# Performance work log

Hardware: AMD Instinct MI355X
Metric: run time of the kernel (lower is better)

The kernel has to match this reference:

```python
import jax, jax.numpy as jnp
import numpy as np
from jax import lax

BN_EPS = 1e-5

def _tern(w):
    # TWN-style ternarization with straight-through estimator
    d = 0.7 * jnp.mean(jnp.abs(w))
    q = jnp.where(jnp.abs(w) > d, jnp.sign(w), jnp.zeros_like(w))
    return w + lax.stop_gradient(q - w)

def _conv(x, w, b):
    y = lax.conv_general_dilated(x, _tern(w), (1, 1), 'SAME',
                                 dimension_numbers=('NCHW', 'OIHW', 'NCHW'))
    return y + b[None, :, None, None]

def _bn4(x, g, b, m, v):
    inv = g * lax.rsqrt(v + BN_EPS)
    return (x - m[None, :, None, None]) * inv[None, :, None, None] + b[None, :, None, None]

def _bn2(x, g, b, m, v):
    return (x - m) * (g * lax.rsqrt(v + BN_EPS)) + b

def _pool(x):
    return lax.reduce_window(x, -jnp.inf, lax.max, (1, 1, 2, 2), (1, 1, 2, 2), 'VALID')


def setup_inputs() -> dict:
    key = jax.random.key(0)
    ks = jax.random.split(key, 8)
    f = jnp.float32
    d = {}
    d['x'] = jax.random.normal(ks[0], (1024, 1, 28, 28), f)
    wshapes = {'w1': (32, 1, 3, 3), 'w2': (64, 32, 3, 3), 'w3': (128, 64, 3, 3),
               'w4': (128, 128, 3, 3), 'wf1': (256, 6272), 'wf2': (128, 256), 'wf3': (10, 128)}
    for i, (n, s) in enumerate(wshapes.items()):
        d[n] = jax.random.normal(ks[i + 1], s, f) * 0.1
    for n, c in [('1', 32), ('2', 64), ('3', 128), ('4', 128)]:
        d['b' + n] = jnp.zeros((c,), f)
        d['g' + n] = jnp.ones((c,), f)
        d['be' + n] = jnp.zeros((c,), f)
        d['m' + n] = jnp.zeros((c,), f)
        d['v' + n] = jnp.ones((c,), f)
    for n, c in [('f1', 256), ('f2', 128)]:
        d['b' + n] = jnp.zeros((c,), f)
        d['g' + n] = jnp.ones((c,), f)
        d['be' + n] = jnp.zeros((c,), f)
        d['m' + n] = jnp.zeros((c,), f)
        d['v' + n] = jnp.ones((c,), f)
    d['bf3'] = jnp.zeros((10,), f)
    return d


def reference(x, w1, b1, g1, be1, m1, v1, w2, b2, g2, be2, m2, v2,
              w3, b3, g3, be3, m3, v3, w4, b4, g4, be4, m4, v4,
              wf1, bf1, gf1, bef1, mf1, vf1, wf2, bf2, gf2, bef2, mf2, vf2,
              wf3, bf3):
    h = jax.nn.relu(_bn4(_conv(x, w1, b1), g1, be1, m1, v1))
    h = jax.nn.relu(_bn4(_conv(h, w2, b2), g2, be2, m2, v2))
    h = _pool(h)                                  # [B,64,14,14]
    h = jax.nn.relu(_bn4(_conv(h, w3, b3), g3, be3, m3, v3))
    h = jax.nn.relu(_bn4(_conv(h, w4, b4), g4, be4, m4, v4))
    h = _pool(h)                                  # [B,128,7,7]
    h = h.reshape(h.shape[0], -1)                 # [B,6272]
    h = jax.nn.relu(_bn2(h @ _tern(wf1).T + bf1, gf1, bef1, mf1, vf1))
    h = jax.nn.relu(_bn2(h @ _tern(wf2).T + bf2, gf2, bef2, mf2, vf2))
    return h @ _tern(wf3).T + bf3                 # [B,10] logits
```

## Files before the change

### kernel.cpp

```cpp
#include <hip/hip_runtime.h>
#include <hip/hip_bf16.h>

#define BN_EPS 1e-5f

typedef __attribute__((ext_vector_type(8))) short bf16x8;
typedef __attribute__((ext_vector_type(4))) float f32x4;
typedef unsigned short u16;
typedef unsigned int u32;

__device__ __forceinline__ void load16(const void* g, void* l) {
    __builtin_amdgcn_global_load_lds((const __attribute__((address_space(1))) void*)g,
                                     (__attribute__((address_space(3))) void*)l, 16, 0, 0);
}
__device__ __forceinline__ u16 f2b(float v) {
    __hip_bfloat16 h = __float2bfloat16(v);
    return *reinterpret_cast<u16*>(&h);
}
__device__ __forceinline__ float ternq(float x, float d) {
    return (fabsf(x) > d) ? (x > 0.f ? 1.f : -1.f) : 0.f;
}

constexpr size_t ALGN(size_t x) { return (x + 255) & ~(size_t)255; }
constexpr size_t O_SUMS = 0;
constexpr size_t O_W1R  = 256;
constexpr size_t O_WF2Q = ALGN(O_W1R + 288 * 4);
constexpr size_t O_WF3Q = ALGN(O_WF2Q + 32768 * 4);
constexpr size_t O_BQ2  = ALGN(O_WF3Q + 1280 * 4);
constexpr size_t O_BQ3  = ALGN(O_BQ2 + 64 * 288 * 2);
constexpr size_t O_BQ4  = ALGN(O_BQ3 + 128 * 576 * 2);
constexpr size_t O_BQF1 = ALGN(O_BQ4 + 128 * 1152 * 2);
constexpr size_t O_F1   = ALGN(O_BQF1 + (size_t)256 * 6272 * 2);
constexpr size_t O_F2   = ALGN(O_F1 + 1024 * 256 * 4);
constexpr size_t O_ACT1 = ALGN(O_F2 + 1024 * 128 * 4);
constexpr size_t O_ACT2 = ALGN(O_ACT1 + (size_t)1024 * 900 * 32 * 2);
constexpr size_t O_ACT3 = ALGN(O_ACT2 + (size_t)1024 * 256 * 64 * 2);
constexpr size_t O_ACT4 = ALGN(O_ACT3 + (size_t)1024 * 256 * 128 * 2);

__global__ void zero_sums(float* s) { if (threadIdx.x < 8) s[threadIdx.x] = 0.f; }

__device__ void absmean_seg(const float* __restrict__ w, int n4, float* __restrict__ sum,
                            int b0, int nb) {
    __shared__ float sm[256];
    float s = 0.f;
    for (int i = b0 * 256 + threadIdx.x; i < n4; i += nb * 256) {
        float4 v = ((const float4*)w)[i];
        s += fabsf(v.x) + fabsf(v.y) + fabsf(v.z) + fabsf(v.w);
    }
    sm[threadIdx.x] = s;
    __syncthreads();
    for (int o = 128; o > 0; o >>= 1) {
        if (threadIdx.x < o) sm[threadIdx.x] += sm[threadIdx.x + o];
        __syncthreads();
    }
    if (threadIdx.x == 0) atomicAdd(sum, sm[0]);
}

__global__ void absmean_all(const float* w1, const float* w2, const float* w3, const float* w4,
                            const float* wf1, const float* wf2, const float* wf3, float* sums) {
    int b = blockIdx.x;
    if (b < 160)      absmean_seg(wf1, 401408, sums + 4, b, 160);
    else if (b < 192) absmean_seg(w4, 36864, sums + 3, b - 160, 32);
    else if (b < 208) absmean_seg(w3, 18432, sums + 2, b - 192, 16);
    else if (b < 216) absmean_seg(w2, 4608, sums + 1, b - 208, 8);
    else if (b < 224) absmean_seg(wf2, 8192, sums + 5, b - 216, 8);
    else if (b < 225) absmean_seg(w1, 72, sums + 0, 0, 1);
    else              absmean_seg(wf3, 320, sums + 6, 0, 1);
}

__device__ void tern_conv_seg(const float* __restrict__ w, float d, u16* __restrict__ bq,
                              int COUT, int CIN, int b0, int nb) {
    int N = COUT * CIN * 9;
    for (int i = b0 * 256 + threadIdx.x; i < N; i += nb * 256) {
        float q = ternq(w[i], d);
        int co = i / (CIN * 9), r = i % (CIN * 9);
        int ci = r / 9, tap = r % 9;
        bq[(size_t)co * CIN * 9 + tap * CIN + ci] = f2b(q);
    }
}
__device__ void tern_conv_prime_seg(const float* __restrict__ w, float d, u16* __restrict__ bqp,
                                    int CIN, int b0, int nb) {
    int N = 128 * CIN * 9;
    for (int i = b0 * 256 + threadIdx.x; i < N; i += nb * 256) {
        float q = ternq(w[i], d);
        int co = i / (CIN * 9), r = i % (CIN * 9);
        int ci = r / 9, tap = r % 9;
        int k = tap * CIN + ci;
        int s = k >> 5, qd = (k & 31) >> 3, e = k & 7;
        int lane = qd * 16 + (co & 15), nt = co >> 4;
        bqp[((size_t)(s * 8 + nt) * 64 + lane) * 8 + e] = f2b(q);
    }
}
__device__ void tern_f32_seg(const float* __restrict__ w, float d, float* __restrict__ wq,
                             int N, int b0, int nb) {
    for (int i = b0 * 256 + threadIdx.x; i < N; i += nb * 256) wq[i] = ternq(w[i], d);
}

__global__ void tern_all(const float* w1, const float* w2, const float* w3, const float* w4,
                         const float* wf1, const float* wf2, const float* wf3,
                         const float* __restrict__ sums,
                         float* w1r, u16* bq2, u16* bq3p, u16* bq4p, u16* bqf1,
                         float* wf2q, float* wf3q) {
    int b = blockIdx.x;
    if (b < 1) {
        tern_f32_seg(w1, 0.7f * sums[0] / 288.f, w1r, 288, 0, 1);
    } else if (b < 9) {
        tern_conv_seg(w2, 0.7f * sums[1] / 18432.f, bq2, 64, 32, b - 1, 8);
    } else if (b < 41) {
        tern_conv_prime_seg(w3, 0.7f * sums[2] / 73728.f, bq3p, 64, b - 9, 32);
    } else if (b < 105) {
        tern_conv_prime_seg(w4, 0.7f * sums[3] / 147456.f, bq4p, 128, b - 41, 64);
    } else if (b < 617) {
        float d = 0.7f * sums[4] / 1605632.f;
        for (int i = (b - 105) * 256 + threadIdx.x; i < 1605632; i += 512 * 256) {
            float q = ternq(wf1[i], d);
            int j = i / 6272, k = i % 6272;
            int c = k / 49, s = k % 49;
            bqf1[(size_t)j * 6272 + s * 128 + c] = f2b(q);
        }
    } else if (b < 633) {
        tern_f32_seg(wf2, 0.7f * sums[5] / 32768.f, wf2q, 32768, b - 617, 16);
    } else {
        tern_f32_seg(wf3, 0.7f * sums[6] / 1280.f, wf3q, 1280, 0, 1);
    }
}

__global__ void zero_f1(float* f1) {
    ((float4*)f1)[blockIdx.x * 256 + threadIdx.x] = make_float4(0.f, 0.f, 0.f, 0.f);
}

__global__ __launch_bounds__(256)
void conv1_direct(const float* __restrict__ x, const float* __restrict__ w1r,
                  const float* __restrict__ bias, const float* __restrict__ gam,
                  const float* __restrict__ bet, const float* __restrict__ mu,
                  const float* __restrict__ var, u16* __restrict__ out) {
    __shared__ float xs[784];
    __shared__ float wsh[288];
    __shared__ float scl[32], sft[32];
    const int n = blockIdx.x, tid = threadIdx.x;
    for (int i = tid; i < 784; i += 256) xs[i] = x[(size_t)n * 784 + i];
    for (int i = tid; i < 288; i += 256) wsh[i] = w1r[i];
    if (tid < 32) {
        float s = gam[tid] * rsqrtf(var[tid] + BN_EPS);
        scl[tid] = s;
        sft[tid] = (bias[tid] - mu[tid]) * s + bet[tid];
    }
    __syncthreads();
    for (int p = tid; p < 784; p += 256) {
        int y = p / 28, xx = p % 28;
        float patch[9];
#pragma unroll
        for (int dy = 0; dy < 3; ++dy)
#pragma unroll
            for (int dx = 0; dx < 3; ++dx) {
                int gy = y + dy - 1, gx = xx + dx - 1;
                patch[dy * 3 + dx] = (gy >= 0 && gy < 28 && gx >= 0 && gx < 28) ? xs[gy * 28 + gx] : 0.f;
            }
        u32 pk[16];
#pragma unroll
        for (int co = 0; co < 32; co += 2) {
            float s0 = 0.f, s1 = 0.f;
#pragma unroll
            for (int t = 0; t < 9; ++t) {
                s0 += wsh[co * 9 + t] * patch[t];
                s1 += wsh[(co + 1) * 9 + t] * patch[t];
            }
            float v0 = fmaxf(s0 * scl[co] + sft[co], 0.f);
            float v1 = fmaxf(s1 * scl[co + 1] + sft[co + 1], 0.f);
            pk[co >> 1] = ((u32)f2b(v1) << 16) | (u32)f2b(v0);
        }
        size_t base = ((size_t)(n * 30 + y + 1) * 30 + (xx + 1)) * 32;
#pragma unroll
        for (int q = 0; q < 4; ++q) ((uint4*)(out + base))[q] = ((uint4*)pk)[q];
    }
}

template<int C, int HP, int HV>
__global__ void border_zero(u16* __restrict__ buf) {
    constexpr int NB = 2 * HP + 2 * HV;
    constexpr int CG = C / 8;
    int i = blockIdx.x * blockDim.x + threadIdx.x;
    if (i >= 1024 * NB * CG) return;
    int cg = i % CG, r = i / CG;
    int b = r % NB, n = r / NB;
    int py, px;
    if (b < HP)               { py = 0;                  px = b; }
    else if (b < 2 * HP)      { py = HP - 1;             px = b - HP; }
    else if (b < 2 * HP + HV) { py = b - 2 * HP + 1;     px = 0; }
    else                      { py = b - 2 * HP - HV + 1; px = HP - 1; }
    size_t off = ((size_t)(n * HP + py) * HP + px) * C + cg * 8;
    *(uint4*)(buf + off) = make_uint4(0, 0, 0, 0);
}

template<int CIN, int BN, int HV, int HP, int G, bool POOL, bool PADOUT>
__global__ __launch_bounds__(256)
void convgemm(const u16* __restrict__ act, const u16* __restrict__ bq,
              const float* __restrict__ bias, const float* __restrict__ gam,
              const float* __restrict__ bet, const float* __restrict__ mu,
              const float* __restrict__ var, u16* __restrict__ out) {
    constexpr int BM = 128;
    constexpr int K = 9 * CIN;
    constexpr int S = K / (32 * G);
    constexpr int TPC = CIN / 32;
    constexpr int NT = BN / 32;
    constexpr int RB = BN / 64;
    constexpr int HO = HV / 2;
    constexpr int PP = POOL ? HO * HO : HV * HV;

    __shared__ __align__(16) u16 Alds[G][BM * 32];
    __shared__ __align__(16) u16 Blds[G][BN * 32];
    __shared__ int rowA[BM];
    __shared__ int rowO[BM];
    __shared__ float scl[BN], sft[BN];

    const int tid = threadIdx.x;
    const int m0 = blockIdx.x * BM;

    for (int t = tid; t < BM; t += 256) {
        int base;
        if (POOL) {
            int p = (m0 >> 2) + (t >> 2), q = t & 3;
            int n = p / PP, rr = p % PP;
            int oy = rr / HO, ox = rr % HO;
            int y = oy * 2 + (q >> 1), x = ox * 2 + (q & 1);
            base = ((n * HP + y) * HP + x) * CIN;
        } else {
            int m = m0 + t;
            int n = m / PP, rr = m % PP;
            int y = rr / HV, x = rr % HV;
            base = ((n * HP + y) * HP + x) * CIN;
        }
        rowA[t] = base;
    }
    if (POOL) {
        if (tid < 32) {
            int p = (m0 >> 2) + tid;
            int n = p / PP, rr = p % PP;
            int oy = rr / HO, ox = rr % HO;
            rowO[tid] = PADOUT ? ((n * 16 + oy + 1) * 16 + ox + 1) * BN : p * BN;
        }
    } else {
        for (int t = tid; t < BM; t += 256) {
            int m = m0 + t;
            int n = m / PP, rr = m % PP;
            int y = rr / HV, x = rr % HV;
            rowO[t] = PADOUT ? ((n * 16 + y + 1) * 16 + x + 1) * BN : m * BN;
        }
    }
    if (tid < BN) {
        float s = gam[tid] * rsqrtf(var[tid] + BN_EPS);
        scl[tid] = s;
        sft[tid] = (bias[tid] - mu[tid]) * s + bet[tid];
    }
    __syncthreads();

    int arow[2];
    arow[0] = rowA[(tid >> 6) * 16 + (tid & 15)];
    arow[1] = rowA[64 + (tid >> 6) * 16 + (tid & 15)];
    const int chunkb = ((tid >> 4) & 3) * 16;
    const int bco = (tid >> 6) * 16 + (tid & 15);
    const char* actb = (const char*)act;
    const char* bqb  = (const char*)bq;

    const int wave = tid >> 6, lane = tid & 63;
    const int wm = wave & 1, wn = wave >> 1;
    const int fr16 = lane * 16;

    f32x4 acc[4][NT] = {};

    for (int s = 0; s < S; ++s) {
#pragma unroll
        for (int j = 0; j < G; ++j) {
            int g = s * G + j;
            int tap = g / TPC, cio = (g % TPC) * 32;
            int dy = tap / 3, dx = tap % 3;
            int toffb = ((dy * HP + dx) * CIN + cio) * 2;
            char* Al = (char*)Alds[j];
#pragma unroll
            for (int r = 0; r < 2; ++r)
                load16(actb + (size_t)arow[r] * 2 + toffb + chunkb, Al + r * 4096 + tid * 16);
            char* Bl = (char*)Blds[j];
            int bkob = g * 64 + chunkb;
#pragma unroll
            for (int r = 0; r < RB; ++r)
                load16(bqb + (size_t)(r * 64 + bco) * K * 2 + bkob, Bl + r * 4096 + tid * 16);
        }
        __syncthreads();
#pragma unroll
        for (int j = 0; j < G; ++j) {
            const char* Al = (const char*)Alds[j];
            const char* Bl = (const char*)Blds[j];
            bf16x8 af[4], bf[NT];
#pragma unroll
            for (int mt = 0; mt < 4; ++mt)
                af[mt] = *(const bf16x8*)(Al + (wm * 4 + mt) * 1024 + fr16);
#pragma unroll
            for (int nt = 0; nt < NT; ++nt)
                bf[nt] = *(const bf16x8*)(Bl + (wn * NT + nt) * 1024 + fr16);
#pragma unroll
            for (int mt = 0; mt < 4; ++mt)
#pragma unroll
                for (int nt = 0; nt < NT; ++nt)
                    acc[mt][nt] = __builtin_amdgcn_mfma_f32_16x16x32_bf16(af[mt], bf[nt], acc[mt][nt], 0, 0, 0);
        }
        __syncthreads();
    }

    const int fr = lane & 15, quad = lane >> 4;
    if (POOL) {
#pragma unroll
        for (int mt = 0; mt < 4; ++mt) {
            int pl = wm * 16 + mt * 4 + quad;
            int ob = rowO[pl];
#pragma unroll
            for (int nt = 0; nt < NT; ++nt) {
                int col = wn * (NT * 16) + nt * 16 + fr;
                float sc = scl[col], sh = sft[col];
                f32x4 a = acc[mt][nt];
                float v0 = a[0] * sc + sh, v1 = a[1] * sc + sh;
                float v2 = a[2] * sc + sh, v3 = a[3] * sc + sh;
                float mx = fmaxf(fmaxf(v0, v1), fmaxf(v2, v3));
                out[(size_t)ob + col] = f2b(fmaxf(mx, 0.f));
            }
        }
    } else {
#pragma unroll
        for (int mt = 0; mt < 4; ++mt) {
            int rb = wm * 64 + mt * 16 + quad * 4;
            int o0 = rowO[rb], o1 = rowO[rb + 1], o2 = rowO[rb + 2], o3 = rowO[rb + 3];
#pragma unroll
            for (int nt = 0; nt < NT; ++nt) {
                int col = wn * (NT * 16) + nt * 16 + fr;
                float sc = scl[col], sh = sft[col];
                f32x4 a = acc[mt][nt];
                out[(size_t)o0 + col] = f2b(fmaxf(a[0] * sc + sh, 0.f));
                out[(size_t)o1 + col] = f2b(fmaxf(a[1] * sc + sh, 0.f));
                out[(size_t)o2 + col] = f2b(fmaxf(a[2] * sc + sh, 0.f));
                out[(size_t)o3 + col] = f2b(fmaxf(a[3] * sc + sh, 0.f));
            }
        }
    }
}

__global__ __launch_bounds__(256)
void conv34(const u16* __restrict__ act2p, const u16* __restrict__ b3p, const u16* __restrict__ b4p,
            const float* __restrict__ b3, const float* __restrict__ g3, const float* __restrict__ be3,
            const float* __restrict__ m3, const float* __restrict__ v3,
            const float* __restrict__ b4, const float* __restrict__ g4, const float* __restrict__ be4,
            const float* __restrict__ m4, const float* __restrict__ v4,
            u16* __restrict__ out) {
    __shared__ __align__(16) u16 Xs[32768];

    const int tid = threadIdx.x;
    const int n = blockIdx.x;
    const int wave = tid >> 6, lane = tid & 63;
    const int wm = wave & 1, wn = wave >> 1;
    const int fr = lane & 15, quad = lane >> 4;
    char* X = (char*)Xs;

    float scl3[4], sft3[4], scl4[4], sft4[4];
#pragma unroll
    for (int nt = 0; nt < 4; ++nt) {
        int c = wn * 64 + nt * 16 + fr;
        float s = g3[c] * rsqrtf(v3[c] + BN_EPS);
        scl3[nt] = s; sft3[nt] = (b3[c] - m3[c]) * s + be3[c];
        s = g4[c] * rsqrtf(v4[c] + BN_EPS);
        scl4[nt] = s; sft4[nt] = (b4[c] - m4[c]) * s + be4[c];
    }

    {
        const uint4* src = (const uint4*)(act2p + (size_t)n * 16384);
#pragma unroll
        for (int it = 0; it < 8; ++it) {
            int i = it * 256 + tid;
            int r = i >> 3, c = i & 7;
            uint4 v = src[i];
            *(uint4*)(X + r * 128 + ((c ^ (r & 7)) * 16)) = v;
        }
    }
    __syncthreads();

    int r0a[7];
#pragma unroll
    for (int mtl = 0; mtl < 7; ++mtl) {
        int g = wm * 7 + mtl + 1;
        int pxc = min(max(fr, 1), 14);
        r0a[mtl] = (g - 1) * 16 + (pxc - 1);
    }
    f32x4 acc[7][4] = {};
    const char* B3 = (const char*)b3p;
#pragma unroll 3
    for (int s = 0; s < 18; ++s) {
        int tap = s >> 1;
        int rdel = (tap / 3) * 16 + tap % 3;
        int cs = (s & 1) * 4;
        bf16x8 af[7], bf[4];
#pragma unroll
        for (int mtl = 0; mtl < 7; ++mtl) {
            int r = r0a[mtl] + rdel;
            int pos = (cs + quad) ^ (r & 7);
            af[mtl] = *(const bf16x8*)(X + r * 128 + pos * 16);
        }
#pragma unroll
        for (int nt = 0; nt < 4; ++nt)
            bf[nt] = *(const bf16x8*)(B3 + ((size_t)((s * 8 + wn * 4 + nt) * 64 + lane)) * 16);
#pragma unroll
        for (int mtl = 0; mtl < 7; ++mtl)
#pragma unroll
            for (int nt = 0; nt < 4; ++nt)
                acc[mtl][nt] = __builtin_amdgcn_mfma_f32_16x16x32_bf16(af[mtl], bf[nt], acc[mtl][nt], 0, 0, 0);
    }
    __syncthreads();

    for (int t = tid; t < 60 * 16; t += 256) {
        int j = t & 15, b = t >> 4;
        int m = (b < 16) ? b : (b < 32) ? 240 + (b - 16) : (b < 46) ? (b - 31) * 16 : (b - 45) * 16 + 15;
        *(uint4*)(X + m * 256 + j * 16) = make_uint4(0, 0, 0, 0);
    }
#pragma unroll
    for (int mtl = 0; mtl < 7; ++mtl) {
        int g = wm * 7 + mtl + 1;
#pragma unroll
        for (int nt = 0; nt < 4; ++nt) {
            int col = wn * 64 + nt * 16 + fr;
            int c = col >> 3;
            f32x4 a = acc[mtl][nt];
#pragma unroll
            for (int j = 0; j < 4; ++j) {
                int px = quad * 4 + j;
                if (px >= 1 && px <= 14) {
                    int m = g * 16 + px;
                    float v = fmaxf(a[j] * scl3[nt] + sft3[nt], 0.f);
                    *(u16*)(X + m * 256 + ((c ^ (m & 15)) * 16) + (col & 7) * 2) = f2b(v);
                }
            }
        }
    }
    __syncthreads();

    int r0b[7];
#pragma unroll
    for (int mtl = 0; mtl < 7; ++mtl) {
        int m = (wm * 7 + mtl) * 16 + fr;
        int p = min(m >> 2, 48), q = m & 3;
        int y2 = (p / 7) * 2 + (q >> 1), x2 = (p % 7) * 2 + (q & 1);
        r0b[mtl] = y2 * 16 + x2;
    }
    f32x4 acc4[7][4] = {};
    const char* B4 = (const char*)b4p;
#pragma unroll 2
    for (int s = 0; s < 36; ++s) {
        int tap = s >> 2;
        int rdel = (tap / 3) * 16 + tap % 3;
        int cs = (s & 3) * 4;
        bf16x8 af[7], bf[4];
#pragma unroll
        for (int mtl = 0; mtl < 7; ++mtl) {
            int r = r0b[mtl] + rdel;
            int pos = (cs + quad) ^ (r & 15);
            af[mtl] = *(const bf16x8*)(X + r * 256 + pos * 16);
        }
#pragma unroll
        for (int nt = 0; nt < 4; ++nt)
            bf[nt] = *(const bf16x8*)(B4 + ((size_t)((s * 8 + wn * 4 + nt) * 64 + lane)) * 16);
#pragma unroll
        for (int mtl = 0; mtl < 7; ++mtl)
#pragma unroll
            for (int nt = 0; nt < 4; ++nt)
                acc4[mtl][nt] = __builtin_amdgcn_mfma_f32_16x16x32_bf16(af[mtl], bf[nt], acc4[mtl][nt], 0, 0, 0);
    }
#pragma unroll
    for (int mtl = 0; mtl < 7; ++mtl) {
        int p = (wm * 7 + mtl) * 4 + quad;
        if (p < 49) {
#pragma unroll
            for (int nt = 0; nt < 4; ++nt) {
                int col = wn * 64 + nt * 16 + fr;
                f32x4 a = acc4[mtl][nt];
                float v0 = a[0] * scl4[nt] + sft4[nt];
                float v1 = a[1] * scl4[nt] + sft4[nt];
                float v2 = a[2] * scl4[nt] + sft4[nt];
                float v3 = a[3] * scl4[nt] + sft4[nt];
                float mx = fmaxf(fmaxf(v0, v1), fmaxf(v2, v3));
                out[((size_t)n * 49 + p) * 128 + col] = f2b(fmaxf(mx, 0.f));
            }
        }
    }
}

__global__ __launch_bounds__(256)
void fc1gemm(const u16* __restrict__ A, const u16* __restrict__ Bq, float* __restrict__ out) {
    constexpr int K = 6272, KC = 896, S = KC / 64;
    __shared__ __align__(16) u16 Alds[2][128 * 32];
    __shared__ __align__(16) u16 Blds[2][128 * 32];
    const int tid = threadIdx.x;
    const int m0 = blockIdx.x * 128;
    const int n0 = blockIdx.y * 128;
    const int k0 = blockIdx.z * KC;
    const int chunkb = ((tid >> 4) & 3) * 16;
    const int rr = (tid >> 6) * 16 + (tid & 15);
    const char* Ag = (const char*)A;
    const char* Bg = (const char*)Bq;
    const int wave = tid >> 6, lane = tid & 63;
    const int wm = wave & 1, wn = wave >> 1;
    const int fr16 = lane * 16;
    f32x4 acc[4][4] = {};

    for (int s = 0; s < S; ++s) {
#pragma unroll
        for (int j = 0; j < 2; ++j) {
            int kb = (k0 + s * 64 + j * 32) * 2 + chunkb;
            char* Al = (char*)Alds[j];
            char* Bl = (char*)Blds[j];
#pragma unroll
            for (int r = 0; r < 2; ++r) {
                load16(Ag + (size_t)(m0 + r * 64 + rr) * K * 2 + kb, Al + r * 4096 + tid * 16);
                load16(Bg + (size_t)(n0 + r * 64 + rr) * K * 2 + kb, Bl + r * 4096 + tid * 16);
            }
        }
        __syncthreads();
#pragma unroll
        for (int j = 0; j < 2; ++j) {
            const char* Al = (const char*)Alds[j];
            const char* Bl = (const char*)Blds[j];
            bf16x8 af[4], bf[4];
#pragma unroll
            for (int mt = 0; mt < 4; ++mt)
                af[mt] = *(const bf16x8*)(Al + (wm * 4 + mt) * 1024 + fr16);
#pragma unroll
            for (int nt = 0; nt < 4; ++nt)
                bf[nt] = *(const bf16x8*)(Bl + (wn * 4 + nt) * 1024 + fr16);
#pragma unroll
            for (int mt = 0; mt < 4; ++mt)
#pragma unroll
                for (int nt = 0; nt < 4; ++nt)
                    acc[mt][nt] = __builtin_amdgcn_mfma_f32_16x16x32_bf16(af[mt], bf[nt], acc[mt][nt], 0, 0, 0);
        }
        __syncthreads();
    }
    const int fr = lane & 15, quad = lane >> 4;
#pragma unroll
    for (int mt = 0; mt < 4; ++mt) {
        int row = m0 + wm * 64 + mt * 16 + quad * 4;
#pragma unroll
        for (int nt = 0; nt < 4; ++nt) {
            int col = n0 + wn * 64 + nt * 16 + fr;
            f32x4 a = acc[mt][nt];
            atomicAdd(&out[(size_t)(row + 0) * 256 + col], a[0]);
            atomicAdd(&out[(size_t)(row + 1) * 256 + col], a[1]);
            atomicAdd(&out[(size_t)(row + 2) * 256 + col], a[2]);
            atomicAdd(&out[(size_t)(row + 3) * 256 + col], a[3]);
        }
    }
}

__global__ __launch_bounds__(256)
void fc2_kernel(const float* __restrict__ A, const float* __restrict__ Bw,
                const float* __restrict__ bA, const float* __restrict__ gA,
                const float* __restrict__ beA, const float* __restrict__ mA,
                const float* __restrict__ vA,
                const float* __restrict__ bias, const float* __restrict__ gam,
                const float* __restrict__ bet, const float* __restrict__ mu,
                const float* __restrict__ var, float* __restrict__ out) {
    constexpr int Nn = 128, K = 256;
    __shared__ __align__(16) float As[16][68];
    __shared__ __align__(16) float Bs[16][68];
    __shared__ float sclA[256], sftA[256];
    const int tid = threadIdx.x;
    const int n0 = blockIdx.x * 64, m0 = blockIdx.y * 64;
    if (tid < 256) {
        float s = gA[tid] * rsqrtf(vA[tid] + BN_EPS);
        sclA[tid] = s;
        sftA[tid] = (bA[tid] - mA[tid]) * s + beA[tid];
    }
    const int tm = tid >> 4, tn = tid & 15;
    const int lr = tid >> 2, lk = (tid & 3) * 4;
    float acc[4][4] = {};
    __syncthreads();
    for (int k0 = 0; k0 < K; k0 += 16) {
        float4 av = *(const float4*)&A[(size_t)(m0 + lr) * K + k0 + lk];
        float4 bv = *(const float4*)&Bw[(size_t)(n0 + lr) * K + k0 + lk];
        As[lk + 0][lr] = fmaxf(av.x * sclA[k0 + lk + 0] + sftA[k0 + lk + 0], 0.f);
        As[lk + 1][lr] = fmaxf(av.y * sclA[k0 + lk + 1] + sftA[k0 + lk + 1], 0.f);
        As[lk + 2][lr] = fmaxf(av.z * sclA[k0 + lk + 2] + sftA[k0 + lk + 2], 0.f);
        As[lk + 3][lr] = fmaxf(av.w * sclA[k0 + lk + 3] + sftA[k0 + lk + 3], 0.f);
        Bs[lk + 0][lr] = bv.x; Bs[lk + 1][lr] = bv.y; Bs[lk + 2][lr] = bv.z; Bs[lk + 3][lr] = bv.w;
        __syncthreads();
#pragma unroll
        for (int k = 0; k < 16; ++k) {
            float4 a = *(const float4*)&As[k][tm * 4];
            float4 b = *(const float4*)&Bs[k][tn * 4];
            acc[0][0] += a.x * b.x; acc[0][1] += a.x * b.y; acc[0][2] += a.x * b.z; acc[0][3] += a.x * b.w;
            acc[1][0] += a.y * b.x; acc[1][1] += a.y * b.y; acc[1][2] += a.y * b.z; acc[1][3] += a.y * b.w;
            acc[2][0] += a.z * b.x; acc[2][1] += a.z * b.y; acc[2][2] += a.z * b.z; acc[2][3] += a.z * b.w;
            acc[3][0] += a.w * b.x; acc[3][1] += a.w * b.y; acc[3][2] += a.w * b.z; acc[3][3] += a.w * b.w;
        }
        __syncthreads();
    }
#pragma unroll
    for (int i = 0; i < 4; ++i) {
        int row = m0 + tm * 4 + i;
#pragma unroll
        for (int j = 0; j < 4; ++j) {
            int col = n0 + tn * 4 + j;
            float sc = gam[col] * rsqrtf(var[col] + BN_EPS);
            float v = (acc[i][j] + bias[col] - mu[col]) * sc + bet[col];
            out[(size_t)row * Nn + col] = fmaxf(v, 0.f);
        }
    }
}

__global__ __launch_bounds__(256)
void fc3_kernel(const float* __restrict__ A, const float* __restrict__ Bw,
                const float* __restrict__ bias, float* __restrict__ out) {
    int i = blockIdx.x * blockDim.x + threadIdx.x;
    if (i >= 1024 * 10) return;
    int n = i / 10, j = i % 10;
    const float4* a = (const float4*)&A[(size_t)n * 128];
    const float4* b = (const float4*)&Bw[(size_t)j * 128];
    float s = 0.f;
#pragma unroll
    for (int k = 0; k < 32; ++k) {
        float4 x = a[k], y = b[k];
        s += x.x * y.x + x.y * y.y + x.z * y.z + x.w * y.w;
    }
    out[i] = s + bias[j];
}

extern "C" void kernel_launch(void* const* d_in, const int* in_sizes, int n_in,
                              void* d_out, int out_size, void* d_ws, size_t ws_size,
                              hipStream_t stream) {
    (void)in_sizes; (void)n_in; (void)out_size; (void)ws_size;
    const float* x   = (const float*)d_in[0];
    const float* w1  = (const float*)d_in[1];
    const float* w2  = (const float*)d_in[2];
    const float* w3  = (const float*)d_in[3];
    const float* w4  = (const float*)d_in[4];
    const float* wf1 = (const float*)d_in[5];
    const float* wf2 = (const float*)d_in[6];
    const float* wf3 = (const float*)d_in[7];
    auto P = [&](int i) { return (const float*)d_in[i]; };
    char* wsb = (char*)d_ws;
    float* sums = (float*)(wsb + O_SUMS);
    float* w1r  = (float*)(wsb + O_W1R);
    float* wf2q = (float*)(wsb + O_WF2Q);
    float* wf3q = (float*)(wsb + O_WF3Q);
    u16* bq2   = (u16*)(wsb + O_BQ2);
    u16* bq3p  = (u16*)(wsb + O_BQ3);
    u16* bq4p  = (u16*)(wsb + O_BQ4);
    u16* bqf1  = (u16*)(wsb + O_BQF1);
    float* f1  = (float*)(wsb + O_F1);
    float* f2  = (float*)(wsb + O_F2);
    u16* act1  = (u16*)(wsb + O_ACT1);
    u16* act2p = (u16*)(wsb + O_ACT2);
    u16* act4p = (u16*)(wsb + O_ACT4);

    zero_sums<<<1, 64, 0, stream>>>(sums);
    absmean_all<<<226, 256, 0, stream>>>(w1, w2, w3, w4, wf1, wf2, wf3, sums);
    tern_all<<<634, 256, 0, stream>>>(w1, w2, w3, w4, wf1, wf2, wf3, sums,
                                      w1r, bq2, bq3p, bq4p, bqf1, wf2q, wf3q);

    border_zero<32, 30, 28><<<(1024 * 116 * 4 + 255) / 256, 256, 0, stream>>>(act1);
    border_zero<64, 16, 14><<<(1024 * 60 * 8 + 255) / 256, 256, 0, stream>>>(act2p);
    zero_f1<<<256, 256, 0, stream>>>(f1);

    conv1_direct<<<1024, 256, 0, stream>>>(x, w1r, P(8), P(9), P(10), P(11), P(12), act1);
    convgemm<32, 64, 28, 30, 1, true, true><<<6272, 256, 0, stream>>>(
        act1, bq2, P(13), P(14), P(15), P(16), P(17), act2p);
    conv34<<<1024, 256, 0, stream>>>(
        act2p, bq3p, bq4p,
        P(18), P(19), P(20), P(21), P(22),
        P(23), P(24), P(25), P(26), P(27), act4p);
    fc1gemm<<<dim3(8, 2, 7), 256, 0, stream>>>(act4p, bqf1, f1);
    fc2_kernel<<<dim3(2, 16), 256, 0, stream>>>(
        f1, wf2q, P(28), P(29), P(30), P(31), P(32),
        P(33), P(34), P(35), P(36), P(37), f2);
    fc3_kernel<<<40, 256, 0, stream>>>(f2, wf3q, P(38), (float*)d_out);
}
```

Before: 417.2 us.

## Restructure conv34 wave tiling to full-N per wave with LDS-based maxpool epilogue

Each wave now owns 64 output rows across all 128 channels (4x8 MFMA tiles) instead of a 2x2 M/N wave split. Conv4 is computed over the full padded 16x16 grid, so the pooled-pixel gather indexing goes away, and the 2x2 max-pool moves to a separate LDS pass using integer max on bf16 bits (valid because values are non-negative after ReLU). The change also adds a two-blocks-per-CU launch bound and moves the BN scale setup next to each epilogue. It aims to cut redundant LDS A-fragment reads and simplify addressing, at the cost of extra MFMA work on padding rows and an added LDS round trip.

```diff
diff --git a/kernel.cpp b/kernel.cpp
--- a/kernel.cpp
+++ b/kernel.cpp
@@ -341,7 +341,7 @@
     }
 }
 
-__global__ __launch_bounds__(256)
+__global__ __launch_bounds__(256, 2)
 void conv34(const u16* __restrict__ act2p, const u16* __restrict__ b3p, const u16* __restrict__ b4p,
             const float* __restrict__ b3, const float* __restrict__ g3, const float* __restrict__ be3,
             const float* __restrict__ m3, const float* __restrict__ v3,
@@ -352,20 +352,9 @@
 
     const int tid = threadIdx.x;
     const int n = blockIdx.x;
-    const int wave = tid >> 6, lane = tid & 63;
-    const int wm = wave & 1, wn = wave >> 1;
+    const int w = tid >> 6, lane = tid & 63;
     const int fr = lane & 15, quad = lane >> 4;
     char* X = (char*)Xs;
-
-    float scl3[4], sft3[4], scl4[4], sft4[4];
-#pragma unroll
-    for (int nt = 0; nt < 4; ++nt) {
-        int c = wn * 64 + nt * 16 + fr;
-        float s = g3[c] * rsqrtf(v3[c] + BN_EPS);
-        scl3[nt] = s; sft3[nt] = (b3[c] - m3[c]) * s + be3[c];
-        s = g4[c] * rsqrtf(v4[c] + BN_EPS);
-        scl4[nt] = s; sft4[nt] = (b4[c] - m4[c]) * s + be4[c];
-    }
 
     {
         const uint4* src = (const uint4*)(act2p + (size_t)n * 16384);
@@ -374,116 +363,157 @@
             int i = it * 256 + tid;
             int r = i >> 3, c = i & 7;
             uint4 v = src[i];
-            *(uint4*)(X + r * 128 + ((c ^ (r & 7)) * 16)) = v;
-        }
-    }
-    __syncthreads();
-
-    int r0a[7];
-#pragma unroll
-    for (int mtl = 0; mtl < 7; ++mtl) {
-        int g = wm * 7 + mtl + 1;
-        int pxc = min(max(fr, 1), 14);
-        r0a[mtl] = (g - 1) * 16 + (pxc - 1);
-    }
-    f32x4 acc[7][4] = {};
+            *(uint4*)(X + r * 128 + ((c ^ (r & 7)) << 4)) = v;
+        }
+    }
+    __syncthreads();
+
+    const int mb = w * 64 + fr;
+    f32x4 acc[4][8];
+#pragma unroll
+    for (int a = 0; a < 4; ++a)
+#pragma unroll
+        for (int b = 0; b < 8; ++b) acc[a][b] = (f32x4){0.f, 0.f, 0.f, 0.f};
+
     const char* B3 = (const char*)b3p;
-#pragma unroll 3
-    for (int s = 0; s < 18; ++s) {
-        int tap = s >> 1;
-        int rdel = (tap / 3) * 16 + tap % 3;
-        int cs = (s & 1) * 4;
-        bf16x8 af[7], bf[4];
-#pragma unroll
-        for (int mtl = 0; mtl < 7; ++mtl) {
-            int r = r0a[mtl] + rdel;
-            int pos = (cs + quad) ^ (r & 7);
-            af[mtl] = *(const bf16x8*)(X + r * 128 + pos * 16);
-        }
-#pragma unroll
-        for (int nt = 0; nt < 4; ++nt)
-            bf[nt] = *(const bf16x8*)(B3 + ((size_t)((s * 8 + wn * 4 + nt) * 64 + lane)) * 16);
-#pragma unroll
-        for (int mtl = 0; mtl < 7; ++mtl)
-#pragma unroll
-            for (int nt = 0; nt < 4; ++nt)
-                acc[mtl][nt] = __builtin_amdgcn_mfma_f32_16x16x32_bf16(af[mtl], bf[nt], acc[mtl][nt], 0, 0, 0);
-    }
-    __syncthreads();
-
-    for (int t = tid; t < 60 * 16; t += 256) {
-        int j = t & 15, b = t >> 4;
-        int m = (b < 16) ? b : (b < 32) ? 240 + (b - 16) : (b < 46) ? (b - 31) * 16 : (b - 45) * 16 + 15;
-        *(uint4*)(X + m * 256 + j * 16) = make_uint4(0, 0, 0, 0);
-    }
-#pragma unroll
-    for (int mtl = 0; mtl < 7; ++mtl) {
-        int g = wm * 7 + mtl + 1;
-#pragma unroll
-        for (int nt = 0; nt < 4; ++nt) {
-            int col = wn * 64 + nt * 16 + fr;
-            int c = col >> 3;
-            f32x4 a = acc[mtl][nt];
+#pragma unroll
+    for (int tap = 0; tap < 9; ++tap) {
+        const int off = (tap / 3 - 1) * 16 + (tap % 3 - 1);
+        int r[4];
+#pragma unroll
+        for (int mt = 0; mt < 4; ++mt) r[mt] = (mb + mt * 16 + off) & 255;
+#pragma unroll
+        for (int h = 0; h < 2; ++h) {
+            const int s = tap * 2 + h;
+            bf16x8 af[4], bf[8];
+#pragma unroll
+            for (int mt = 0; mt < 4; ++mt) {
+                int pos = (h * 4 + quad) ^ (r[mt] & 7);
+                af[mt] = *(const bf16x8*)(X + r[mt] * 128 + pos * 16);
+            }
+#pragma unroll
+            for (int nt = 0; nt < 8; ++nt)
+                bf[nt] = *(const bf16x8*)(B3 + (size_t)((s * 8 + nt) * 64 + lane) * 16);
+#pragma unroll
+            for (int mt = 0; mt < 4; ++mt)
+#pragma unroll
+                for (int nt = 0; nt < 8; ++nt)
+                    acc[mt][nt] = __builtin_amdgcn_mfma_f32_16x16x32_bf16(af[mt], bf[nt], acc[mt][nt], 0, 0, 0);
+        }
+    }
+    __syncthreads();
+
+    {
+        float scl3[8], sft3[8];
+#pragma unroll
+        for (int nt = 0; nt < 8; ++nt) {
+            int c = nt * 16 + fr;
+            float s = g3[c] * rsqrtf(v3[c] + BN_EPS);
+            scl3[nt] = s;
+            sft3[nt] = (b3[c] - m3[c]) * s + be3[c];
+        }
+        for (int t = tid; t < 960; t += 256) {
+            int ch = t & 15, b = t >> 4;
+            int m = (b < 16) ? b : (b < 32) ? 224 + b : (b < 46) ? (b - 31) * 16 : (b - 45) * 16 + 15;
+            *(uint4*)(X + m * 256 + ((ch ^ (m & 15)) << 4)) = make_uint4(0, 0, 0, 0);
+        }
+#pragma unroll
+        for (int mt = 0; mt < 4; ++mt) {
+            int y = w * 4 + mt;
+            if (y >= 1 && y <= 14) {
+#pragma unroll
+                for (int j = 0; j < 4; ++j) {
+                    int x = quad * 4 + j;
+                    if (x >= 1 && x <= 14) {
+                        int m = y * 16 + x;
+#pragma unroll
+                        for (int nt = 0; nt < 8; ++nt) {
+                            int col = nt * 16 + fr;
+                            float v = fmaxf(acc[mt][nt][j] * scl3[nt] + sft3[nt], 0.f);
+                            *(u16*)(X + m * 256 + (((col >> 3) ^ (m & 15)) << 4) + (col & 7) * 2) = f2b(v);
+                        }
+                    }
+                }
+            }
+        }
+    }
+    __syncthreads();
+
+#pragma unroll
+    for (int a = 0; a < 4; ++a)
+#pragma unroll
+        for (int b = 0; b < 8; ++b) acc[a][b] = (f32x4){0.f, 0.f, 0.f, 0.f};
+    const char* B4 = (const char*)b4p;
+#pragma unroll
+    for (int tap = 0; tap < 9; ++tap) {
+        const int off = (tap / 3 - 1) * 16 + (tap % 3 - 1);
+        int r[4];
+#pragma unroll
+        for (int mt = 0; mt < 4; ++mt) r[mt] = (mb + mt * 16 + off) & 255;
+#pragma unroll
+        for (int qr = 0; qr < 4; ++qr) {
+            const int s = tap * 4 + qr;
+            bf16x8 af[4], bf[8];
+#pragma unroll
+            for (int mt = 0; mt < 4; ++mt) {
+                int pos = (qr * 4 + quad) ^ (r[mt] & 15);
+                af[mt] = *(const bf16x8*)(X + r[mt] * 256 + pos * 16);
+            }
+#pragma unroll
+            for (int nt = 0; nt < 8; ++nt)
+                bf[nt] = *(const bf16x8*)(B4 + (size_t)((s * 8 + nt) * 64 + lane) * 16);
+#pragma unroll
+            for (int mt = 0; mt < 4; ++mt)
+#pragma unroll
+                for (int nt = 0; nt < 8; ++nt)
+                    acc[mt][nt] = __builtin_amdgcn_mfma_f32_16x16x32_bf16(af[mt], bf[nt], acc[mt][nt], 0, 0, 0);
+        }
+    }
+    __syncthreads();
+
+    {
+        float scl4[8], sft4[8];
+#pragma unroll
+        for (int nt = 0; nt < 8; ++nt) {
+            int c = nt * 16 + fr;
+            float s = g4[c] * rsqrtf(v4[c] + BN_EPS);
+            scl4[nt] = s;
+            sft4[nt] = (b4[c] - m4[c]) * s + be4[c];
+        }
+#pragma unroll
+        for (int mt = 0; mt < 4; ++mt) {
 #pragma unroll
             for (int j = 0; j < 4; ++j) {
-                int px = quad * 4 + j;
-                if (px >= 1 && px <= 14) {
-                    int m = g * 16 + px;
-                    float v = fmaxf(a[j] * scl3[nt] + sft3[nt], 0.f);
-                    *(u16*)(X + m * 256 + ((c ^ (m & 15)) * 16) + (col & 7) * 2) = f2b(v);
+                int m = w * 64 + mt * 16 + quad * 4 + j;
+#pragma unroll
+                for (int nt = 0; nt < 8; ++nt) {
+                    int col = nt * 16 + fr;
+                    float v = fmaxf(acc[mt][nt][j] * scl4[nt] + sft4[nt], 0.f);
+                    *(u16*)(X + m * 256 + (((col >> 3) ^ (m & 15)) << 4) + (col & 7) * 2) = f2b(v);
                 }
             }
         }
     }
     __syncthreads();
 
-    int r0b[7];
-#pragma unroll
-    for (int mtl = 0; mtl < 7; ++mtl) {
-        int m = (wm * 7 + mtl) * 16 + fr;
-        int p = min(m >> 2, 48), q = m & 3;
-        int y2 = (p / 7) * 2 + (q >> 1), x2 = (p % 7) * 2 + (q & 1);
-        r0b[mtl] = y2 * 16 + x2;
-    }
-    f32x4 acc4[7][4] = {};
-    const char* B4 = (const char*)b4p;
-#pragma unroll 2
-    for (int s = 0; s < 36; ++s) {
-        int tap = s >> 2;
-        int rdel = (tap / 3) * 16 + tap % 3;
-        int cs = (s & 3) * 4;
-        bf16x8 af[7], bf[4];
-#pragma unroll
-        for (int mtl = 0; mtl < 7; ++mtl) {
-            int r = r0b[mtl] + rdel;
-            int pos = (cs + quad) ^ (r & 15);
-            af[mtl] = *(const bf16x8*)(X + r * 256 + pos * 16);
-        }
-#pragma unroll
-        for (int nt = 0; nt < 4; ++nt)
-            bf[nt] = *(const bf16x8*)(B4 + ((size_t)((s * 8 + wn * 4 + nt) * 64 + lane)) * 16);
-#pragma unroll
-        for (int mtl = 0; mtl < 7; ++mtl)
-#pragma unroll
-            for (int nt = 0; nt < 4; ++nt)
-                acc4[mtl][nt] = __builtin_amdgcn_mfma_f32_16x16x32_bf16(af[mtl], bf[nt], acc4[mtl][nt], 0, 0, 0);
-    }
-#pragma unroll
-    for (int mtl = 0; mtl < 7; ++mtl) {
-        int p = (wm * 7 + mtl) * 4 + quad;
-        if (p < 49) {
-#pragma unroll
-            for (int nt = 0; nt < 4; ++nt) {
-                int col = wn * 64 + nt * 16 + fr;
-                f32x4 a = acc4[mtl][nt];
-                float v0 = a[0] * scl4[nt] + sft4[nt];
-                float v1 = a[1] * scl4[nt] + sft4[nt];
-                float v2 = a[2] * scl4[nt] + sft4[nt];
-                float v3 = a[3] * scl4[nt] + sft4[nt];
-                float mx = fmaxf(fmaxf(v0, v1), fmaxf(v2, v3));
-                out[((size_t)n * 49 + p) * 128 + col] = f2b(fmaxf(mx, 0.f));
-            }
-        }
+    for (int t = tid; t < 784; t += 256) {
+        int ch = t & 15, p = t >> 4;
+        int oy = p / 7, ox = p % 7;
+        int r00 = (2 * oy + 1) * 16 + (2 * ox + 1);
+        int r01 = r00 + 1, r10 = r00 + 16, r11 = r00 + 17;
+        uint4 A0 = *(const uint4*)(X + r00 * 256 + ((ch ^ (r00 & 15)) << 4));
+        uint4 A1 = *(const uint4*)(X + r01 * 256 + ((ch ^ (r01 & 15)) << 4));
+        uint4 A2 = *(const uint4*)(X + r10 * 256 + ((ch ^ (r10 & 15)) << 4));
+        uint4 A3 = *(const uint4*)(X + r11 * 256 + ((ch ^ (r11 & 15)) << 4));
+        const u16* pa = (const u16*)&A0;
+        const u16* pb = (const u16*)&A1;
+        const u16* pc = (const u16*)&A2;
+        const u16* pd = (const u16*)&A3;
+        u16 o[8];
+#pragma unroll
+        for (int e = 0; e < 8; ++e)
+            o[e] = (u16)max(max((int)pa[e], (int)pb[e]), max((int)pc[e], (int)pd[e]));
+        *(uint4*)(out + ((size_t)n * 49 + p) * 128 + ch * 8) = *(const uint4*)o;
     }
 }
 
```

Result: slower. 714.7 us (+71.3%).
